# Optimization experiments

Hardware: AMD Instinct MI355X
Metric: run time of the kernel (lower is better)

## Reference

```python
import jax, jax.numpy as jnp
import numpy as np

HEADS = 4
AGENT = 49  # 7x7 agent tokens
LN_EPS = 1e-5


def setup_inputs() -> dict:
    key = jax.random.key(0)
    ks = jax.random.split(key, 3)
    B, C, H, W = 2, 128, 56, 56
    x = jax.random.normal(ks[0], (B, C, H, W), jnp.float32)
    # 1x1 convs == per-pixel linear maps; store as [out_ch, in_ch]
    w_qkv = jax.random.normal(ks[1], (3 * C, C), jnp.float32) * (C ** -0.5)
    w_proj = jax.random.normal(ks[2], (C, C), jnp.float32) * (C ** -0.5)
    b_proj = jnp.zeros((C,), jnp.float32)
    ln_g = jnp.ones((C,), jnp.float32)
    ln_b = jnp.zeros((C,), jnp.float32)
    return {"x": x, "w_qkv": w_qkv, "w_proj": w_proj, "b_proj": b_proj,
            "ln_g": ln_g, "ln_b": ln_b}


def reference(x, w_qkv, w_proj, b_proj, ln_g, ln_b):
    B, C, H, W = x.shape
    heads = HEADS
    hd = C // heads
    N = H * W
    scale = hd ** -0.5
    a = int(AGENT ** 0.5)  # 7; H,W divisible by a -> exact adaptive avg pool

    # 1x1-conv QKV: [B,3C,H,W] -> [B,3,heads,hd,N] -> q,k,v [B,h,N,hd]
    qkv = jnp.einsum('oc,bchw->bohw', w_qkv, x).reshape(B, 3, heads, hd, N)
    q = jnp.transpose(qkv[:, 0], (0, 1, 3, 2))
    k = jnp.transpose(qkv[:, 1], (0, 1, 3, 2))
    v = jnp.transpose(qkv[:, 2], (0, 1, 3, 2))

    # agent tokens: adaptive avg pool to (a,a) == uniform block mean
    agent = x.reshape(B, C, a, H // a, a, W // a).mean(axis=(3, 5))  # [B,C,a,a]
    agent = agent.reshape(B, heads, hd, AGENT)
    agent = jnp.transpose(agent, (0, 1, 3, 2))  # [B,h,A,hd]

    # stage 1: compress q through agent tokens
    q_to_agent = jax.nn.softmax(
        jnp.einsum('bhnd,bhad->bhna', q * scale, agent), axis=-1)  # [B,h,N,A]
    q_compressed = jnp.einsum('bhna,bhad->bhnd', q_to_agent, agent)  # [B,h,N,hd]

    # stage 2: full N x N attention with compressed queries
    attn = jax.nn.softmax(
        jnp.einsum('bhnd,bhmd->bhnm', q_compressed * scale, k), axis=-1)
    out = jnp.einsum('bhnm,bhmd->bhnd', attn, v)  # [B,h,N,hd]

    # merge heads -> [B,N,C], 1x1-conv proj, LayerNorm over C
    out = jnp.transpose(out, (0, 2, 1, 3)).reshape(B, N, C)
    out = jnp.einsum('bnc,oc->bno', out, w_proj) + b_proj
    mu = out.mean(-1, keepdims=True)
    var = out.var(-1, keepdims=True)
    out = (out - mu) / jnp.sqrt(var + LN_EPS) * ln_g + ln_b
    return jnp.transpose(out.reshape(B, H, W, C), (0, 3, 1, 2))
```

## Files before the change

kernel.cpp:

```cpp
#include <hip/hip_runtime.h>
#include <hip/hip_bf16.h>
#include <stdint.h>

typedef unsigned short u16;
typedef __attribute__((ext_vector_type(8))) short short8;
typedef __attribute__((ext_vector_type(4))) short short4v;
typedef __attribute__((ext_vector_type(4))) float f32x4;

#define NB 2
#define NC 128
#define NHD 4
#define HD 32
#define NN 3136
#define NA 49
#define NSPLIT 4
#define NKP 3200
#define NTILE 25
#define SCALE 0.17677669529663687f
#define LOG2E 1.4426950408889634f
#define QSC (SCALE * LOG2E)

__device__ inline u16 bfb(float f) {
    __hip_bfloat16 h = __float2bfloat16(f);
    return *(u16*)&h;
}
__device__ inline float b2f(u16 w) {
    return __uint_as_float(((uint32_t)w) << 16);
}
__device__ inline short4v pack4(float a, float b, float c, float d) {
    union { short4v s; __hip_bfloat162 h[2]; } u;
    u.h[0] = __float22bfloat162_rn(make_float2(a, b));
    u.h[1] = __float22bfloat162_rn(make_float2(c, d));
    return u.s;
}
__device__ inline float ldf(const void* p, size_t i, int f) {
    return f ? b2f(((const u16*)p)[i]) : ((const float*)p)[i];
}
__device__ inline void gld16(const u16* g, u16* l) {
    __builtin_amdgcn_global_load_lds(
        (__attribute__((address_space(1))) void*)(g),
        (__attribute__((address_space(3))) void*)(l), 16, 0, 0);
}
__device__ inline void stage8k(const u16* g, u16* lds, int w, int lane) {
    gld16(g + (size_t)(w * 64 + lane) * 8,       lds + (size_t)w * 512);
    gld16(g + (size_t)(256 + w * 64 + lane) * 8, lds + 2048 + (size_t)w * 512);
}
__device__ inline int detect_local(const u16* raw, int t) {
    __shared__ int cnt;
    if (t == 0) cnt = 0;
    __syncthreads();
    float a = fabsf(b2f(raw[t * 97]));
    if (a >= 1e-4f && a <= 100.0f) atomicAdd(&cnt, 1);
    __syncthreads();
    return cnt >= 230;
}

__global__ __launch_bounds__(256) void k_prep(const void* __restrict__ xr,
                                              const void* __restrict__ wq,
                                              const void* __restrict__ wp,
                                              const void* __restrict__ bp,
                                              const void* __restrict__ g,
                                              const void* __restrict__ bb,
                                              u16* __restrict__ xTs,
                                              u16* __restrict__ wbf,
                                              u16* __restrict__ wps,
                                              float* __restrict__ bgb,
                                              u16* __restrict__ agb,
                                              u16* __restrict__ agT,
                                              int* __restrict__ flagOut) {
    __shared__ u16 tile[128][18];
    int bx = blockIdx.x, t = threadIdx.x;
    int f = detect_local((const u16*)xr, t);
    if (bx < 392) {
        int b = bx / 196;
        int n0 = (bx % 196) * 16;
        int T = n0 >> 6, nbase = n0 & 63;
        int c = t >> 1, nh = (t & 1) * 8;
        size_t src = ((size_t)(b * 128 + c)) * NN + n0 + nh;
#pragma unroll
        for (int i = 0; i < 8; ++i) tile[c][nh + i] = bfb(ldf(xr, src + i, f));
        __syncthreads();
        int n = t >> 4, ktu = t & 15;
        int c0 = ktu * 8;
        short8 o;
#pragma unroll
        for (int i = 0; i < 8; ++i) o[i] = (short)tile[c0 + i][n];
        *(short8*)&xTs[(((size_t)b * 49 + T) * 16 + ktu) * 512 + (nbase + n) * 8] = o;
    } else if (bx < 584) {
        int i = (bx - 392) * 256 + t;
        wbf[i] = bfb(ldf(wq, i, f));
    } else if (bx < 648) {
        int i = (bx - 584) * 256 + t;
        int o = i >> 7, c = i & 127;
        int otile = o >> 4, oloc = o & 15, ktu = c >> 3, wi = c & 7;
        wps[((otile * 16 + ktu) * 16 + oloc) * 8 + wi] = bfb(ldf(wp, i, f));
    } else if (bx < 650) {
        int i = (bx - 648) * 256 + t;
        if (i < 128)      bgb[i] = ldf(bp, i, f);
        else if (i < 256) bgb[i] = ldf(g, i - 128, f);
        else if (i < 384) bgb[i] = ldf(bb, i - 256, f);
        if (bx == 648 && t == 0) *flagOut = f;
    } else {
        int idx = (bx - 650) * 256 + t;
        const int NPOOL = NB * NC * NA;
        if (idx < NPOOL) {
            int b = idx / (NC * NA);
            int r = idx % (NC * NA);
            int c = r / NA;
            int a = r % NA;
            int ai = a / 7, aj = a % 7;
            size_t base = ((size_t)(b * NC + c)) * NN + ai * 8 * 56 + aj * 8;
            float s = 0.f;
            if (f) {
                const u16* xp = (const u16*)xr + base;
#pragma unroll
                for (int uu = 0; uu < 8; ++uu) {
                    ushort4 a0 = *(const ushort4*)&xp[uu * 56];
                    ushort4 a1 = *(const ushort4*)&xp[uu * 56 + 4];
                    s += b2f(a0.x) + b2f(a0.y) + b2f(a0.z) + b2f(a0.w)
                       + b2f(a1.x) + b2f(a1.y) + b2f(a1.z) + b2f(a1.w);
                }
            } else {
                const float* xp = (const float*)xr + base;
#pragma unroll
                for (int uu = 0; uu < 8; ++uu) {
                    float4 v0 = *(const float4*)&xp[uu * 56];
                    float4 v1 = *(const float4*)&xp[uu * 56 + 4];
                    s += v0.x + v0.y + v0.z + v0.w + v1.x + v1.y + v1.z + v1.w;
                }
            }
            int h = c >> 5, d = c & 31;
            int bh = b * NHD + h;
            u16 val = bfb(s * (1.f / 64.f));
            agb[bh * 2048 + a * 32 + d] = val;
            agT[bh * 2048 + d * 64 + a] = val;
        } else {
            int j = idx - NPOOL;
            if (j < 3840) {
                int bh = j / 480, rem = j % 480;
                int a = 49 + rem / 32, d = rem % 32;
                agb[bh * 2048 + a * 32 + d] = 0;
            } else if (j < 7680) {
                j -= 3840;
                int bh = j / 480, rem = j % 480;
                int a = 49 + rem / 32, d = rem % 32;
                agT[bh * 2048 + d * 64 + a] = 0;
            }
        }
    }
}

__global__ __launch_bounds__(256, 4) void k_qkv_s1(const u16* __restrict__ xTs,
                                                   const u16* __restrict__ wbf,
                                                   const u16* __restrict__ agb,
                                                   const u16* __restrict__ agT,
                                                   u16* __restrict__ kbf,
                                                   u16* __restrict__ vtb,
                                                   u16* __restrict__ qcb) {
    __shared__ __align__(16) u16 xs[8192];
    __shared__ u16 qtile[2 * 64 * 40];
    int b = blockIdx.z;
    int n0 = blockIdx.x * 64;
    int w = threadIdx.x >> 6, lane = threadIdx.x & 63;
    int c = lane & 15, u = lane >> 4;
    int t = threadIdx.x;
    const u16* xtile = xTs + (((size_t)b * 49 + (n0 >> 6)) * 16) * 512;
#pragma unroll
    for (int i = 0; i < 4; ++i)
        gld16(xtile + (size_t)(i * 256 + t) * 8, xs + (size_t)(i * 256 + t) * 8);
    int o0 = blockIdx.y * 64 + w * 16;
    const f32x4 z = {0.f, 0.f, 0.f, 0.f};
    short8 af0 = *(const short8*)&wbf[(o0 + c) * 128 +  0 + u * 8];
    short8 af1 = *(const short8*)&wbf[(o0 + c) * 128 + 32 + u * 8];
    short8 af2 = *(const short8*)&wbf[(o0 + c) * 128 + 64 + u * 8];
    short8 af3 = *(const short8*)&wbf[(o0 + c) * 128 + 96 + u * 8];
    int tq = o0 >> 7, h = (o0 >> 5) & 3, d0 = (o0 & 31) + u * 4;
    size_t bh = (size_t)b * NHD + h;
    __syncthreads();
#pragma unroll
    for (int nt = 0; nt < 4; ++nt) {
        int n = n0 + nt * 16 + c;
        f32x4 acc = z;
        acc = __builtin_amdgcn_mfma_f32_16x16x32_bf16(af0,
            *(const short8*)&xs[((0 * 4 + u) * 64 + nt * 16 + c) * 8], acc, 0, 0, 0);
        acc = __builtin_amdgcn_mfma_f32_16x16x32_bf16(af1,
            *(const short8*)&xs[((1 * 4 + u) * 64 + nt * 16 + c) * 8], acc, 0, 0, 0);
        acc = __builtin_amdgcn_mfma_f32_16x16x32_bf16(af2,
            *(const short8*)&xs[((2 * 4 + u) * 64 + nt * 16 + c) * 8], acc, 0, 0, 0);
        acc = __builtin_amdgcn_mfma_f32_16x16x32_bf16(af3,
            *(const short8*)&xs[((3 * 4 + u) * 64 + nt * 16 + c) * 8], acc, 0, 0, 0);
        if (tq == 0) {
            int hl = (o0 >> 5) & 1;
            *(short4v*)&qtile[(hl * 64 + nt * 16 + c) * 40 + d0] =
                pack4(acc[0] * QSC, acc[1] * QSC, acc[2] * QSC, acc[3] * QSC);
        } else if (tq == 1) {
            int tile = n >> 7, sub = (n >> 4) & 7, key = n & 15;
            int dg = d0 >> 3, wi = d0 & 7;
            size_t kb0 = (((size_t)bh * NTILE + tile) * 8 + sub) * 4 + dg;
            *(short4v*)&kbf[kb0 * 128 + key * 8 + wi] =
                pack4(acc[0], acc[1], acc[2], acc[3]);
        } else {
            int tile = n >> 7, kt2 = n & 127;
            int sub = kt2 >> 4, uu = (kt2 >> 2) & 3, jj = n & 3;
            size_t vb0 = ((size_t)bh * NTILE + tile) * 4096 + sub * 512 + uu * 128 + jj;
#pragma unroll
            for (int r = 0; r < 4; ++r)
                vtb[vb0 + (d0 + r) * 4] = bfb(acc[r]);
        }
    }
    if (blockIdx.y < 2) {
        __syncthreads();
#pragma unroll
        for (int tt = w; tt < 8; tt += 4) {
            int hl2 = tt >> 2, r0 = (tt & 3) * 16;
            int hg = blockIdx.y * 2 + hl2;
            size_t bh2 = (size_t)b * NHD + hg;
            const u16* aB = agb + bh2 * 2048;
            const u16* aT = agT + bh2 * 2048;
            short8 qf = *(const short8*)&qtile[(hl2 * 64 + r0 + c) * 40 + u * 8];
            f32x4 st[4];
#pragma unroll
            for (int t2 = 0; t2 < 4; ++t2) {
                short8 afr = *(const short8*)&aB[(t2 * 16 + c) * 32 + u * 8];
                st[t2] = __builtin_amdgcn_mfma_f32_16x16x32_bf16(afr, qf, z, 0, 0, 0);
            }
            float e[4][4];
            float lsum = 0.f;
#pragma unroll
            for (int t2 = 0; t2 < 4; ++t2)
#pragma unroll
                for (int r = 0; r < 4; ++r) {
                    float v = __builtin_amdgcn_exp2f(st[t2][r]);
                    if (t2 == 3 && !(u == 0 && r == 0)) v = 0.f;
                    e[t2][r] = v;
                    lsum += v;
                }
            lsum += __shfl_xor(lsum, 16);
            lsum += __shfl_xor(lsum, 32);
            float linv = 1.f / lsum;
            f32x4 qlo = z, qhi = z;
#pragma unroll
            for (int t2 = 0; t2 < 4; ++t2) {
                short4v pf = pack4(e[t2][0] * linv, e[t2][1] * linv,
                                   e[t2][2] * linv, e[t2][3] * linv);
                short4v alo = *(const short4v*)&aT[c * 64 + t2 * 16 + u * 4];
                short4v ahi = *(const short4v*)&aT[(c + 16) * 64 + t2 * 16 + u * 4];
                qlo = __builtin_amdgcn_mfma_f32_16x16x16bf16_1k(alo, pf, qlo, 0, 0, 0);
                qhi = __builtin_amdgcn_mfma_f32_16x16x16bf16_1k(ahi, pf, qhi, 0, 0, 0);
            }
            u16* dst = &qcb[(bh2 * NN + n0 + r0 + c) * HD];
            *(short4v*)&dst[u * 4]      = pack4(qlo[0] * QSC, qlo[1] * QSC, qlo[2] * QSC, qlo[3] * QSC);
            *(short4v*)&dst[16 + u * 4] = pack4(qhi[0] * QSC, qhi[1] * QSC, qhi[2] * QSC, qhi[3] * QSC);
        }
    }
}

__global__ __launch_bounds__(256, 3) void k_flash4(const u16* __restrict__ qc,
                                                   const u16* __restrict__ kb,
                                                   const u16* __restrict__ vt,
                                                   u16* __restrict__ opb,
                                                   float* __restrict__ lp) {
    __shared__ __align__(16) u16 Ks[2][4096];
    __shared__ __align__(16) u16 Vs[2][4096];
    int b = blockIdx.z;
    int h = blockIdx.y & 3;
    int s = blockIdx.y >> 2;
    int w = threadIdx.x >> 6, lane = threadIdx.x & 63;
    int c = lane & 15, u = lane >> 4;
    int qa = blockIdx.x * 128 + w * 32;
    int qbr = qa + 16;
    if (qa  > NN - 16) qa  = NN - 16;
    if (qbr > NN - 16) qbr = NN - 16;
    size_t bh = (size_t)b * NHD + h;
    const u16* kg = kb + bh * (size_t)NTILE * 4096;
    const u16* vg = vt + bh * (size_t)NTILE * 4096;
    short8 qfA = *(const short8*)(qc + (bh * NN + qa  + c) * HD + u * 8);
    short8 qfB = *(const short8*)(qc + (bh * NN + qbr + c) * HD + u * 8);
    const f32x4 z = {0.f, 0.f, 0.f, 0.f};
    f32x4 oA0 = z, oA1 = z, oB0 = z, oB1 = z;
    float lA = 0.f, lB = 0.f;
    int t0 = (s * NTILE) / NSPLIT, t1 = ((s + 1) * NTILE) / NSPLIT;
    stage8k(kg + (size_t)t0 * 4096, &Ks[0][0], w, lane);
    stage8k(vg + (size_t)t0 * 4096, &Vs[0][0], w, lane);
#pragma unroll 1
    for (int t = t0; t < t1; ++t) {
        int buf = (t - t0) & 1;
        __syncthreads();
        if (t + 1 < t1) {
            stage8k(kg + (size_t)(t + 1) * 4096, &Ks[buf ^ 1][0], w, lane);
            stage8k(vg + (size_t)(t + 1) * 4096, &Vs[buf ^ 1][0], w, lane);
        }
        const u16* kp = &Ks[buf][0];
        const u16* vp = &Vs[buf][0];
        int kk = t * 128;
        bool tail = (kk + 128 > NN);
#pragma unroll
        for (int sub = 0; sub < 8; ++sub) {
            short8 kf = *(const short8*)(kp + ((sub * 4 + u) * 16 + c) * 8);
            f32x4 sA = __builtin_amdgcn_mfma_f32_16x16x32_bf16(kf, qfA, z, 0, 0, 0);
            f32x4 sB = __builtin_amdgcn_mfma_f32_16x16x32_bf16(kf, qfB, z, 0, 0, 0);
            float eA[4], eB[4];
#pragma unroll
            for (int r = 0; r < 4; ++r) {
                eA[r] = __builtin_amdgcn_exp2f(sA[r]);
                eB[r] = __builtin_amdgcn_exp2f(sB[r]);
            }
            if (tail) {
#pragma unroll
                for (int r = 0; r < 4; ++r)
                    if (kk + sub * 16 + u * 4 + r >= NN) { eA[r] = 0.f; eB[r] = 0.f; }
            }
            lA += (eA[0] + eA[1]) + (eA[2] + eA[3]);
            lB += (eB[0] + eB[1]) + (eB[2] + eB[3]);
            short4v pA = pack4(eA[0], eA[1], eA[2], eA[3]);
            short4v pB = pack4(eB[0], eB[1], eB[2], eB[3]);
            short4v va = *(const short4v*)(vp + sub * 512 + u * 128 + c * 4);
            short4v vb = *(const short4v*)(vp + sub * 512 + u * 128 + (c + 16) * 4);
            oA0 = __builtin_amdgcn_mfma_f32_16x16x16bf16_1k(va, pA, oA0, 0, 0, 0);
            oA1 = __builtin_amdgcn_mfma_f32_16x16x16bf16_1k(vb, pA, oA1, 0, 0, 0);
            oB0 = __builtin_amdgcn_mfma_f32_16x16x16bf16_1k(va, pB, oB0, 0, 0, 0);
            oB1 = __builtin_amdgcn_mfma_f32_16x16x16bf16_1k(vb, pB, oB1, 0, 0, 0);
        }
    }
    lA += __shfl_xor(lA, 16); lA += __shfl_xor(lA, 32);
    lB += __shfl_xor(lB, 16); lB += __shfl_xor(lB, 32);
    float iA = 1.f / lA, iB = 1.f / lB;
    u16* oba = opb + (((size_t)(s * NB + b)) * NN + qa + c) * NC + h * HD;
    *(short4v*)&oba[u * 4]      = pack4(oA0[0] * iA, oA0[1] * iA, oA0[2] * iA, oA0[3] * iA);
    *(short4v*)&oba[16 + u * 4] = pack4(oA1[0] * iA, oA1[1] * iA, oA1[2] * iA, oA1[3] * iA);
    u16* obb = opb + (((size_t)(s * NB + b)) * NN + qbr + c) * NC + h * HD;
    *(short4v*)&obb[u * 4]      = pack4(oB0[0] * iB, oB0[1] * iB, oB0[2] * iB, oB0[3] * iB);
    *(short4v*)&obb[16 + u * 4] = pack4(oB1[0] * iB, oB1[1] * iB, oB1[2] * iB, oB1[3] * iB);
    if (u == 0) {
        lp[(((size_t)(s * NB + b)) * NHD + h) * NN + qa  + c] = lA;
        lp[(((size_t)(s * NB + b)) * NHD + h) * NN + qbr + c] = lB;
    }
}

__global__ __launch_bounds__(256, 4) void k_proj2(const u16* __restrict__ opb,
                                                  const float* __restrict__ lp,
                                                  const u16* __restrict__ wps,
                                                  const float* __restrict__ bgb,
                                                  void* __restrict__ out,
                                                  const int* __restrict__ flag) {
    __shared__ __align__(16) u16 wl[16384];
    __shared__ u16 Af[16 * 136];
    __shared__ float red1[4][16], red2[4][16];
    int bx = blockIdx.x;
    int b = bx >= 196;
    int n0 = (bx - b * 196) * 16;
    int t = threadIdx.x;
#pragma unroll
    for (int i = 0; i < 8; ++i)
        gld16(wps + (size_t)(i * 256 + t) * 8, wl + (size_t)(i * 256 + t) * 8);
    {
        int row = t >> 4, c8 = (t & 15) * 8;
        int n = n0 + row;
        int hh = c8 >> 5;
        float num[8] = {};
        float den = 0.f;
#pragma unroll
        for (int s = 0; s < NSPLIT; ++s) {
            float ls = lp[(((size_t)(s * NB + b)) * NHD + hh) * NN + n];
            short8 o8 = *(const short8*)&opb[(((size_t)(s * NB + b)) * NN + n) * NC + c8];
            den += ls;
#pragma unroll
            for (int i = 0; i < 8; ++i) num[i] += ls * b2f((u16)o8[i]);
        }
        float inv = 1.f / den;
        u16* dst = &Af[row * 136 + c8];
#pragma unroll
        for (int i = 0; i < 8; i += 2) {
            __hip_bfloat162 p = __float22bfloat162_rn(
                make_float2(num[i] * inv, num[i + 1] * inv));
            *(uint32_t*)&dst[i] = *(uint32_t*)&p;
        }
    }
    __syncthreads();
    int w = t >> 6, lane = t & 63, c = lane & 15, u = lane >> 4;
    int oA = w * 32 + c, oB = w * 32 + 16 + c;
    const f32x4 z = {0.f, 0.f, 0.f, 0.f};
    f32x4 cA = z, cB = z;
#pragma unroll
    for (int kf = 0; kf < 4; ++kf) {
        short8 a  = *(const short8*)&Af[c * 136 + kf * 32 + u * 8];
        short8 bA = *(const short8*)&wl[(((2 * w) * 16 + kf * 4 + u) * 16 + c) * 8];
        short8 bB = *(const short8*)&wl[(((2 * w + 1) * 16 + kf * 4 + u) * 16 + c) * 8];
        cA = __builtin_amdgcn_mfma_f32_16x16x32_bf16(a, bA, cA, 0, 0, 0);
        cB = __builtin_amdgcn_mfma_f32_16x16x32_bf16(a, bB, cB, 0, 0, 0);
    }
    float bpA = bgb[oA], bpB = bgb[oB];
    float s1[4], s2[4];
#pragma unroll
    for (int r = 0; r < 4; ++r) {
        cA[r] += bpA; cB[r] += bpB;
        s1[r] = cA[r] + cB[r];
        s2[r] = cA[r] * cA[r] + cB[r] * cB[r];
    }
#pragma unroll
    for (int off = 1; off < 16; off <<= 1)
#pragma unroll
        for (int r = 0; r < 4; ++r) {
            s1[r] += __shfl_xor(s1[r], off);
            s2[r] += __shfl_xor(s2[r], off);
        }
    if (c == 0)
#pragma unroll
        for (int r = 0; r < 4; ++r) {
            red1[w][u * 4 + r] = s1[r];
            red2[w][u * 4 + r] = s2[r];
        }
    __syncthreads();
    float gA = bgb[128 + oA], beA = bgb[256 + oA];
    float gB = bgb[128 + oB], beB = bgb[256 + oB];
    float outA[4], outB[4];
#pragma unroll
    for (int r = 0; r < 4; ++r) {
        int row = u * 4 + r;
        float S1 = (red1[0][row] + red1[1][row]) + (red1[2][row] + red1[3][row]);
        float S2 = (red2[0][row] + red2[1][row]) + (red2[2][row] + red2[3][row]);
        float mu = S1 * (1.f / NC);
        float ex = S2 * (1.f / NC);
        float rstd = rsqrtf(ex - mu * mu + 1e-5f);
        outA[r] = (cA[r] - mu) * rstd * gA + beA;
        outB[r] = (cB[r] - mu) * rstd * gB + beB;
    }
    int n = n0 + u * 4;
    if (*flag) {
        __hip_bfloat16* ob = (__hip_bfloat16*)out;
        ushort4 sA = make_ushort4(bfb(outA[0]), bfb(outA[1]), bfb(outA[2]), bfb(outA[3]));
        ushort4 sB = make_ushort4(bfb(outB[0]), bfb(outB[1]), bfb(outB[2]), bfb(outB[3]));
        *(ushort4*)&ob[((size_t)(b * NC + oA)) * NN + n] = sA;
        *(ushort4*)&ob[((size_t)(b * NC + oB)) * NN + n] = sB;
    } else {
        float* ob = (float*)out;
        *(float4*)&ob[((size_t)(b * NC + oA)) * NN + n] = make_float4(outA[0], outA[1], outA[2], outA[3]);
        *(float4*)&ob[((size_t)(b * NC + oB)) * NN + n] = make_float4(outB[0], outB[1], outB[2], outB[3]);
    }
}

extern "C" void kernel_launch(void* const* d_in, const int* in_sizes, int n_in,
                              void* d_out, int out_size, void* d_ws, size_t ws_size,
                              hipStream_t stream) {
    const void* x_raw  = d_in[0];
    const void* wq_raw = d_in[1];
    const void* wp_raw = d_in[2];
    const void* bp_raw = d_in[3];
    const void* lg_raw = d_in[4];
    const void* lb_raw = d_in[5];

    float* ws   = (float*)d_ws;
    int*   flag = (int*)d_ws;
    float* bgb  = ws + 16;
    float* lp   = bgb + 512;
    u16*   opb  = (u16*)(lp + (size_t)NSPLIT * NB * NHD * NN);
    u16*   xTs  = opb + (size_t)NSPLIT * NB * NN * NC;
    u16*   wbf  = xTs + (size_t)NB * NN * NC;
    u16*   wps  = wbf + 3 * NC * NC;
    u16*   kbf  = wps + NC * NC;
    u16*   vtb  = kbf + (size_t)NB * NHD * NTILE * 4096;
    u16*   qcb  = vtb + (size_t)NB * NHD * NTILE * 4096;
    u16*   agb  = qcb + (size_t)NB * NHD * NN * HD;
    u16*   agT  = agb + NB * NHD * 64 * 32;

    k_prep<<<729, 256, 0, stream>>>(x_raw, wq_raw, wp_raw, bp_raw, lg_raw, lb_raw,
                                    xTs, wbf, wps, bgb, agb, agT, flag);
    k_qkv_s1<<<dim3(NN / 64, 6, NB), 256, 0, stream>>>(xTs, wbf, agb, agT,
                                                       kbf, vtb, qcb);
    k_flash4<<<dim3(25, NHD * NSPLIT, NB), 256, 0, stream>>>(qcb, kbf, vtb, opb, lp);
    k_proj2<<<392, 256, 0, stream>>>(opb, lp, wps, bgb, d_out, flag);
}
```

Measured before the change: 115.5 us.

## Fuse x transpose and weight conversion into QKV kernel; MFMA row-sum in flash

Measured after the change: 113.3 us. No clear change (-1.9%).

```diff
diff --git a/kernel.cpp b/kernel.cpp
--- a/kernel.cpp
+++ b/kernel.cpp
@@ -14,7 +14,6 @@
 #define NN 3136
 #define NA 49
 #define NSPLIT 4
-#define NKP 3200
 #define NTILE 25
 #define SCALE 0.17677669529663687f
 #define LOG2E 1.4426950408889634f
@@ -33,6 +32,14 @@
     u.h[1] = __float22bfloat162_rn(make_float2(c, d));
     return u.s;
 }
+__device__ inline short8 pack8(float4 a, float4 b) {
+    union { short8 s; __hip_bfloat162 h[4]; } u;
+    u.h[0] = __float22bfloat162_rn(make_float2(a.x, a.y));
+    u.h[1] = __float22bfloat162_rn(make_float2(a.z, a.w));
+    u.h[2] = __float22bfloat162_rn(make_float2(b.x, b.y));
+    u.h[3] = __float22bfloat162_rn(make_float2(b.z, b.w));
+    return u.s;
+}
 __device__ inline float ldf(const void* p, size_t i, int f) {
     return f ? b2f(((const u16*)p)[i]) : ((const float*)p)[i];
 }
@@ -56,52 +63,30 @@
 }
 
 __global__ __launch_bounds__(256) void k_prep(const void* __restrict__ xr,
-                                              const void* __restrict__ wq,
                                               const void* __restrict__ wp,
                                               const void* __restrict__ bp,
                                               const void* __restrict__ g,
                                               const void* __restrict__ bb,
-                                              u16* __restrict__ xTs,
-                                              u16* __restrict__ wbf,
                                               u16* __restrict__ wps,
                                               float* __restrict__ bgb,
                                               u16* __restrict__ agb,
                                               u16* __restrict__ agT,
                                               int* __restrict__ flagOut) {
-    __shared__ u16 tile[128][18];
     int bx = blockIdx.x, t = threadIdx.x;
     int f = detect_local((const u16*)xr, t);
-    if (bx < 392) {
-        int b = bx / 196;
-        int n0 = (bx % 196) * 16;
-        int T = n0 >> 6, nbase = n0 & 63;
-        int c = t >> 1, nh = (t & 1) * 8;
-        size_t src = ((size_t)(b * 128 + c)) * NN + n0 + nh;
-#pragma unroll
-        for (int i = 0; i < 8; ++i) tile[c][nh + i] = bfb(ldf(xr, src + i, f));
-        __syncthreads();
-        int n = t >> 4, ktu = t & 15;
-        int c0 = ktu * 8;
-        short8 o;
-#pragma unroll
-        for (int i = 0; i < 8; ++i) o[i] = (short)tile[c0 + i][n];
-        *(short8*)&xTs[(((size_t)b * 49 + T) * 16 + ktu) * 512 + (nbase + n) * 8] = o;
-    } else if (bx < 584) {
-        int i = (bx - 392) * 256 + t;
-        wbf[i] = bfb(ldf(wq, i, f));
-    } else if (bx < 648) {
-        int i = (bx - 584) * 256 + t;
+    if (bx < 64) {
+        int i = bx * 256 + t;
         int o = i >> 7, c = i & 127;
-        int otile = o >> 4, oloc = o & 15, ktu = c >> 3, wi = c & 7;
-        wps[((otile * 16 + ktu) * 16 + oloc) * 8 + wi] = bfb(ldf(wp, i, f));
-    } else if (bx < 650) {
-        int i = (bx - 648) * 256 + t;
+        wps[(((o >> 4) * 16 + (c >> 3)) * 16 + (o & 15)) * 8 + (c & 7)] =
+            bfb(ldf(wp, i, f));
+    } else if (bx < 66) {
+        int i = (bx - 64) * 256 + t;
         if (i < 128)      bgb[i] = ldf(bp, i, f);
         else if (i < 256) bgb[i] = ldf(g, i - 128, f);
         else if (i < 384) bgb[i] = ldf(bb, i - 256, f);
-        if (bx == 648 && t == 0) *flagOut = f;
+        if (bx == 64 && t == 0) *flagOut = f;
     } else {
-        int idx = (bx - 650) * 256 + t;
+        int idx = (bx - 66) * 256 + t;
         const int NPOOL = NB * NC * NA;
         if (idx < NPOOL) {
             int b = idx / (NC * NA);
@@ -150,44 +135,85 @@
     }
 }
 
-__global__ __launch_bounds__(256, 4) void k_qkv_s1(const u16* __restrict__ xTs,
-                                                   const u16* __restrict__ wbf,
+__global__ __launch_bounds__(256, 4) void k_qkv_s1(const void* __restrict__ xr,
+                                                   const void* __restrict__ wq,
                                                    const u16* __restrict__ agb,
                                                    const u16* __restrict__ agT,
                                                    u16* __restrict__ kbf,
                                                    u16* __restrict__ vtb,
                                                    u16* __restrict__ qcb) {
     __shared__ __align__(16) u16 xs[8192];
-    __shared__ u16 qtile[2 * 64 * 40];
-    int b = blockIdx.z;
+    __shared__ __align__(16) u16 tmpq[8320];
+    u16* qtile = tmpq;
+    int t = threadIdx.x;
+    int f = detect_local((const u16*)xr, t);
+    int B = blockIdx.z;
     int n0 = blockIdx.x * 64;
-    int w = threadIdx.x >> 6, lane = threadIdx.x & 63;
+    const f32x4 z = {0.f, 0.f, 0.f, 0.f};
+    {
+        int c = t >> 1, half = t & 1;
+        size_t base = ((size_t)(B * 128 + c)) * NN + n0 + half * 32;
+        u16 vals[32];
+        if (f) {
+            const u16* xp = (const u16*)xr + base;
+#pragma unroll
+            for (int j = 0; j < 4; ++j) {
+                short8 v = *(const short8*)&xp[j * 8];
+#pragma unroll
+                for (int e = 0; e < 8; ++e) vals[j * 8 + e] = (u16)v[e];
+            }
+        } else {
+            const float* xp = (const float*)xr + base;
+#pragma unroll
+            for (int j = 0; j < 8; ++j) {
+                float4 v = *(const float4*)&xp[j * 4];
+                vals[j * 4 + 0] = bfb(v.x); vals[j * 4 + 1] = bfb(v.y);
+                vals[j * 4 + 2] = bfb(v.z); vals[j * 4 + 3] = bfb(v.w);
+            }
+        }
+#pragma unroll
+        for (int i = 0; i < 32; ++i)
+            tmpq[c * 65 + half * 32 + i] = vals[i];
+    }
+    __syncthreads();
+#pragma unroll
+    for (int k = 0; k < 4; ++k) {
+        int j = k * 256 + t;
+        int gg = j >> 6, n = j & 63;
+        short8 o;
+#pragma unroll
+        for (int ci = 0; ci < 8; ++ci) o[ci] = (short)tmpq[(gg * 8 + ci) * 65 + n];
+        *(short8*)&xs[(size_t)j * 8] = o;
+    }
+    int w = t >> 6, lane = t & 63;
     int c = lane & 15, u = lane >> 4;
-    int t = threadIdx.x;
-    const u16* xtile = xTs + (((size_t)b * 49 + (n0 >> 6)) * 16) * 512;
-#pragma unroll
-    for (int i = 0; i < 4; ++i)
-        gld16(xtile + (size_t)(i * 256 + t) * 8, xs + (size_t)(i * 256 + t) * 8);
     int o0 = blockIdx.y * 64 + w * 16;
-    const f32x4 z = {0.f, 0.f, 0.f, 0.f};
-    short8 af0 = *(const short8*)&wbf[(o0 + c) * 128 +  0 + u * 8];
-    short8 af1 = *(const short8*)&wbf[(o0 + c) * 128 + 32 + u * 8];
-    short8 af2 = *(const short8*)&wbf[(o0 + c) * 128 + 64 + u * 8];
-    short8 af3 = *(const short8*)&wbf[(o0 + c) * 128 + 96 + u * 8];
+    short8 af[4];
+    if (f) {
+        const u16* wqp = (const u16*)wq + (size_t)(o0 + c) * 128 + u * 8;
+#pragma unroll
+        for (int kt = 0; kt < 4; ++kt) af[kt] = *(const short8*)&wqp[kt * 32];
+    } else {
+        const float* wqp = (const float*)wq + (size_t)(o0 + c) * 128 + u * 8;
+#pragma unroll
+        for (int kt = 0; kt < 4; ++kt)
+            af[kt] = pack8(*(const float4*)&wqp[kt * 32],
+                           *(const float4*)&wqp[kt * 32 + 4]);
+    }
     int tq = o0 >> 7, h = (o0 >> 5) & 3, d0 = (o0 & 31) + u * 4;
-    size_t bh = (size_t)b * NHD + h;
+    size_t bh = (size_t)B * NHD + h;
     __syncthreads();
 #pragma unroll
     for (int nt = 0; nt < 4; ++nt) {
         int n = n0 + nt * 16 + c;
         f32x4 acc = z;
-        acc = __builtin_amdgcn_mfma_f32_16x16x32_bf16(af0,
+        acc = __builtin_amdgcn_mfma_f32_16x16x32_bf16(af[0],
             *(const short8*)&xs[((0 * 4 + u) * 64 + nt * 16 + c) * 8], acc, 0, 0, 0);
-        acc = __builtin_amdgcn_mfma_f32_16x16x32_bf16(af1,
+        acc = __builtin_amdgcn_mfma_f32_16x16x32_bf16(af[1],
             *(const short8*)&xs[((1 * 4 + u) * 64 + nt * 16 + c) * 8], acc, 0, 0, 0);
-        acc = __builtin_amdgcn_mfma_f32_16x16x32_bf16(af2,
+        acc = __builtin_amdgcn_mfma_f32_16x16x32_bf16(af[2],
             *(const short8*)&xs[((2 * 4 + u) * 64 + nt * 16 + c) * 8], acc, 0, 0, 0);
-        acc = __builtin_amdgcn_mfma_f32_16x16x32_bf16(af3,
+        acc = __builtin_amdgcn_mfma_f32_16x16x32_bf16(af[3],
             *(const short8*)&xs[((3 * 4 + u) * 64 + nt * 16 + c) * 8], acc, 0, 0, 0);
         if (tq == 0) {
             int hl = (o0 >> 5) & 1;
@@ -214,7 +240,7 @@
         for (int tt = w; tt < 8; tt += 4) {
             int hl2 = tt >> 2, r0 = (tt & 3) * 16;
             int hg = blockIdx.y * 2 + hl2;
-            size_t bh2 = (size_t)b * NHD + hg;
+            size_t bh2 = (size_t)B * NHD + hg;
             const u16* aB = agb + bh2 * 2048;
             const u16* aT = agT + bh2 * 2048;
             short8 qf = *(const short8*)&qtile[(hl2 * 64 + r0 + c) * 40 + u * 8];
@@ -277,8 +303,11 @@
     short8 qfA = *(const short8*)(qc + (bh * NN + qa  + c) * HD + u * 8);
     short8 qfB = *(const short8*)(qc + (bh * NN + qbr + c) * HD + u * 8);
     const f32x4 z = {0.f, 0.f, 0.f, 0.f};
+    short4v ones4;
+#pragma unroll
+    for (int i = 0; i < 4; ++i) ones4[i] = (short)0x3F80;
     f32x4 oA0 = z, oA1 = z, oB0 = z, oB1 = z;
-    float lA = 0.f, lB = 0.f;
+    f32x4 lAa = z, lBa = z;
     int t0 = (s * NTILE) / NSPLIT, t1 = ((s + 1) * NTILE) / NSPLIT;
     stage8k(kg + (size_t)t0 * 4096, &Ks[0][0], w, lane);
     stage8k(vg + (size_t)t0 * 4096, &Vs[0][0], w, lane);
@@ -310,8 +339,6 @@
                 for (int r = 0; r < 4; ++r)
                     if (kk + sub * 16 + u * 4 + r >= NN) { eA[r] = 0.f; eB[r] = 0.f; }
             }
-            lA += (eA[0] + eA[1]) + (eA[2] + eA[3]);
-            lB += (eB[0] + eB[1]) + (eB[2] + eB[3]);
             short4v pA = pack4(eA[0], eA[1], eA[2], eA[3]);
             short4v pB = pack4(eB[0], eB[1], eB[2], eB[3]);
             short4v va = *(const short4v*)(vp + sub * 512 + u * 128 + c * 4);
@@ -320,10 +347,11 @@
             oA1 = __builtin_amdgcn_mfma_f32_16x16x16bf16_1k(vb, pA, oA1, 0, 0, 0);
             oB0 = __builtin_amdgcn_mfma_f32_16x16x16bf16_1k(va, pB, oB0, 0, 0, 0);
             oB1 = __builtin_amdgcn_mfma_f32_16x16x16bf16_1k(vb, pB, oB1, 0, 0, 0);
-        }
-    }
-    lA += __shfl_xor(lA, 16); lA += __shfl_xor(lA, 32);
-    lB += __shfl_xor(lB, 16); lB += __shfl_xor(lB, 32);
+            lAa = __builtin_amdgcn_mfma_f32_16x16x16bf16_1k(ones4, pA, lAa, 0, 0, 0);
+            lBa = __builtin_amdgcn_mfma_f32_16x16x16bf16_1k(ones4, pB, lBa, 0, 0, 0);
+        }
+    }
+    float lA = lAa[0], lB = lBa[0];
     float iA = 1.f / lA, iB = 1.f / lB;
     u16* oba = opb + (((size_t)(s * NB + b)) * NN + qa + c) * NC + h * HD;
     *(short4v*)&oba[u * 4]      = pack4(oA0[0] * iA, oA0[1] * iA, oA0[2] * iA, oA0[3] * iA);
@@ -449,23 +477,20 @@
     const void* lg_raw = d_in[4];
     const void* lb_raw = d_in[5];
 
-    float* ws   = (float*)d_ws;
     int*   flag = (int*)d_ws;
-    float* bgb  = ws + 16;
+    float* bgb  = (float*)d_ws + 16;
     float* lp   = bgb + 512;
     u16*   opb  = (u16*)(lp + (size_t)NSPLIT * NB * NHD * NN);
-    u16*   xTs  = opb + (size_t)NSPLIT * NB * NN * NC;
-    u16*   wbf  = xTs + (size_t)NB * NN * NC;
-    u16*   wps  = wbf + 3 * NC * NC;
+    u16*   wps  = opb + (size_t)NSPLIT * NB * NN * NC;
     u16*   kbf  = wps + NC * NC;
     u16*   vtb  = kbf + (size_t)NB * NHD * NTILE * 4096;
     u16*   qcb  = vtb + (size_t)NB * NHD * NTILE * 4096;
     u16*   agb  = qcb + (size_t)NB * NHD * NN * HD;
     u16*   agT  = agb + NB * NHD * 64 * 32;
 
-    k_prep<<<729, 256, 0, stream>>>(x_raw, wq_raw, wp_raw, bp_raw, lg_raw, lb_raw,
-                                    xTs, wbf, wps, bgb, agb, agT, flag);
-    k_qkv_s1<<<dim3(NN / 64, 6, NB), 256, 0, stream>>>(xTs, wbf, agb, agT,
+    k_prep<<<145, 256, 0, stream>>>(x_raw, wp_raw, bp_raw, lg_raw, lb_raw,
+                                    wps, bgb, agb, agT, flag);
+    k_qkv_s1<<<dim3(NN / 64, 6, NB), 256, 0, stream>>>(x_raw, wq_raw, agb, agT,
                                                        kbf, vtb, qcb);
     k_flash4<<<dim3(25, NHD * NSPLIT, NB), 256, 0, stream>>>(qcb, kbf, vtb, opb, lp);
     k_proj2<<<392, 256, 0, stream>>>(opb, lp, wps, bgb, d_out, flag);
```
